# Kernel tuning notes

Hardware: AMD Instinct MI355X
Metric: run time of the kernel (lower is better)

## Reference

```python
import jax, jax.numpy as jnp
import numpy as np

B, N, C, H, W_, K, POS = 1, 100000, 128, 256, 256, 4, 36


def setup_inputs() -> dict:
    key = jax.random.key(0)
    ks = jax.random.split(key, 12)
    inp = {}
    # query coords in [-1, 1] (grid_sample normalized space)
    inp["query"] = jax.random.uniform(ks[0], (B, N, 3), jnp.float32, -1.0, 1.0)
    inp["pe"] = jax.random.normal(ks[1], (B, N, POS), jnp.float32)
    for i, p in enumerate(["xy", "xz", "yz"]):
        inp[f"feat_{p}"] = jax.random.normal(ks[2 + i], (B, C, H, W_), jnp.float32)
        inp[f"Wa_{p}"] = jax.random.normal(ks[5 + i], (POS, K), jnp.float32) * 0.1
        inp[f"ba_{p}"] = jnp.zeros((K,), jnp.float32)
        # offsets initialized to zero in the module; use small random so sampling is non-trivial
        inp[f"Wo_{p}"] = jax.random.normal(ks[8 + i], (POS, 2 * K), jnp.float32) * 0.02
        inp[f"bo_{p}"] = jnp.zeros((2 * K,), jnp.float32)
    return inp


def _bilinear_border(feat, gx, gy):
    """F.grid_sample(feat, grid, align_corners=False, padding_mode='border').
    feat: [B,C,H,W]; gx,gy: [B,N,K] normalized x (width) and y (height) coords.
    Returns [B,C,N,K]."""
    b, c, h, w = feat.shape
    # unnormalize (align_corners=False) then border-clip
    x = jnp.clip(((gx + 1.0) * w - 1.0) * 0.5, 0.0, w - 1.0)
    y = jnp.clip(((gy + 1.0) * h - 1.0) * 0.5, 0.0, h - 1.0)
    x0 = jnp.floor(x)
    y0 = jnp.floor(y)
    wx = x - x0  # [B,N,K]
    wy = y - y0
    xi0 = x0.astype(jnp.int32)
    yi0 = y0.astype(jnp.int32)
    xi1 = jnp.minimum(xi0 + 1, w - 1)
    yi1 = jnp.minimum(yi0 + 1, h - 1)
    ff = feat.reshape(b, c, h * w)
    gather = jax.vmap(lambda f, lin: f[:, lin])  # [C,HW],[N,K] -> [C,N,K]
    v00 = gather(ff, yi0 * w + xi0)
    v01 = gather(ff, yi0 * w + xi1)
    v10 = gather(ff, yi1 * w + xi0)
    v11 = gather(ff, yi1 * w + xi1)
    wx_ = wx[:, None]
    wy_ = wy[:, None]
    return (v00 * (1.0 - wx_) * (1.0 - wy_) + v01 * wx_ * (1.0 - wy_)
            + v10 * (1.0 - wx_) * wy_ + v11 * wx_ * wy_)


def _sample_plane(coords, pe, feat, Wa, ba, Wo, bo):
    b, n, _ = coords.shape
    attn = jax.nn.softmax(pe @ Wa + ba, axis=-1)            # [B,N,K]
    off = (pe @ Wo + bo).reshape(b, n, K, 2)                 # [B,N,K,2]
    sc = coords[:, :, None, :] + off                         # [B,N,K,2]
    # torch code flips last dim before grid_sample: grid x = sc[...,1], y = sc[...,0]
    sampled = _bilinear_border(feat, sc[..., 1], sc[..., 0])  # [B,C,N,K]
    out = jnp.einsum('bcnk,bnk->bnc', sampled, attn)         # weighted sum over K
    return out


def reference(query, pe, feat_xy, feat_xz, feat_yz,
              Wa_xy, ba_xy, Wo_xy, bo_xy,
              Wa_xz, ba_xz, Wo_xz, bo_xz,
              Wa_yz, ba_yz, Wo_yz, bo_yz):
    idx_xy = jnp.array([0, 1])
    idx_xz = jnp.array([0, 2])
    idx_yz = jnp.array([1, 2])
    f_xy = _sample_plane(query[..., idx_xy], pe, feat_xy, Wa_xy, ba_xy, Wo_xy, bo_xy)
    f_xz = _sample_plane(query[..., idx_xz], pe, feat_xz, Wa_xz, ba_xz, Wo_xz, bo_xz)
    f_yz = _sample_plane(query[..., idx_yz], pe, feat_yz, Wa_yz, ba_yz, Wo_yz, bo_yz)
    return f_xy + f_xz + f_yz
```

## Files before the change

kernel.cpp:

```cpp
#include <hip/hip_runtime.h>
#include <hip/hip_fp16.h>
#include <math.h>

#define NQ   100000
#define CCH  128
#define HDIM 256
#define WDIM 256
#define HW   (HDIM * WDIM)
#define KPTS 4
#define PDIM 36
#define NBIN 32768
#define RECW 40

__device__ inline int axis_bin(float x) {
  int b = (int)((x + 1.0f) * 16.0f);
  return min(31, max(0, b));
}
__device__ inline unsigned int spread5(unsigned int x) {
  return (x & 1u) | ((x & 2u) << 2) | ((x & 4u) << 4) | ((x & 8u) << 6) | ((x & 16u) << 8);
}
__device__ inline unsigned int bin_of(float x, float y, float z) {
  return spread5((unsigned int)axis_bin(x)) |
         (spread5((unsigned int)axis_bin(y)) << 1) |
         (spread5((unsigned int)axis_bin(z)) << 2);
}

__global__ void transpose_kernel(const float* __restrict__ f0,
                                 const float* __restrict__ f1,
                                 const float* __restrict__ f2,
                                 __half2* __restrict__ out) {
  __shared__ float tile[64][65];
  const int plane = blockIdx.z;
  const float* __restrict__ f = (plane == 0) ? f0 : ((plane == 1) ? f1 : f2);
  __half2* __restrict__ o = out + (size_t)plane * (size_t)HW * (CCH / 2);
  const int hw0 = blockIdx.x * 64;
  const int c0 = blockIdx.y * 64;
  const int t = threadIdx.x;
  const int c_l = t >> 6;
  const int hw_l = t & 63;
#pragma unroll
  for (int i = 0; i < 16; ++i) {
    tile[c_l + 4 * i][hw_l] = f[(size_t)(c0 + c_l + 4 * i) * HW + (hw0 + hw_l)];
  }
  __syncthreads();
#pragma unroll
  for (int i = 0; i < 8; ++i) {
    const int idx = t + 256 * i;
    const int j = idx & 31;
    const int r = idx >> 5;
    o[(size_t)(hw0 + r) * (CCH / 2) + (c0 / 2 + j)] =
        __floats2half2_rn(tile[2 * j][r], tile[2 * j + 1][r]);
  }
}

__global__ void hist_kernel(const float* __restrict__ query,
                            unsigned int* __restrict__ counts) {
  const int q = blockIdx.x * 256 + threadIdx.x;
  if (q >= NQ) return;
  const unsigned int b = bin_of(query[q * 3 + 0], query[q * 3 + 1], query[q * 3 + 2]);
  atomicAdd(&counts[b], 1u);
}

__global__ void scan_kernel(const unsigned int* __restrict__ counts,
                            unsigned int* __restrict__ offs) {
  __shared__ unsigned int s[1024];
  const int t = threadIdx.x;
  unsigned int c[32];
  unsigned int sum = 0;
  const int base_i = t * 32;
#pragma unroll
  for (int j = 0; j < 32; ++j) { c[j] = counts[base_i + j]; sum += c[j]; }
  s[t] = sum;
  __syncthreads();
  for (int d = 1; d < 1024; d <<= 1) {
    const unsigned int v = (t >= d) ? s[t - d] : 0u;
    __syncthreads();
    s[t] += v;
    __syncthreads();
  }
  unsigned int run = s[t] - sum;
#pragma unroll
  for (int j = 0; j < 32; ++j) { offs[base_i + j] = run; run += c[j]; }
}

__global__ void scatter_kernel(const float* __restrict__ query,
                               unsigned int* __restrict__ offs,
                               unsigned int* __restrict__ perm) {
  const int q = blockIdx.x * 256 + threadIdx.x;
  if (q >= NQ) return;
  const unsigned int b = bin_of(query[q * 3 + 0], query[q * 3 + 1], query[q * 3 + 2]);
  const unsigned int pos = atomicAdd(&offs[b], 1u);
  perm[pos] = (unsigned int)q;
}

__global__ void weights_kernel(const float* __restrict__ query,
                               const float* __restrict__ pe,
                               const unsigned int* __restrict__ perm,
                               const float* __restrict__ Wa0, const float* __restrict__ ba0,
                               const float* __restrict__ Wo0, const float* __restrict__ bo0,
                               const float* __restrict__ Wa1, const float* __restrict__ ba1,
                               const float* __restrict__ Wo1, const float* __restrict__ bo1,
                               const float* __restrict__ Wa2, const float* __restrict__ ba2,
                               const float* __restrict__ Wo2, const float* __restrict__ bo2,
                               unsigned int* __restrict__ rec) {
  __shared__ float sWa[3][PDIM][4];
  __shared__ float sWo[3][PDIM][8];
  __shared__ float sba[3][4];
  __shared__ float sbo[3][8];
  const int t = threadIdx.x;
  {
    float* wa = &sWa[0][0][0];
    for (int i = t; i < 144; i += 256) { wa[i] = Wa0[i]; wa[144 + i] = Wa1[i]; wa[288 + i] = Wa2[i]; }
    float* wo = &sWo[0][0][0];
    for (int i = t; i < 288; i += 256) { wo[i] = Wo0[i]; wo[288 + i] = Wo1[i]; wo[576 + i] = Wo2[i]; }
    if (t < 4) { sba[0][t] = ba0[t]; sba[1][t] = ba1[t]; sba[2][t] = ba2[t]; }
    if (t < 8) { sbo[0][t] = bo0[t]; sbo[1][t] = bo1[t]; sbo[2][t] = bo2[t]; }
  }
  __syncthreads();

  const int n = blockIdx.x * 256 + t;
  if (n >= NQ) return;
  const int q = (int)perm[n];

  float p[PDIM];
  const float4* pe4 = (const float4*)(pe + (size_t)q * PDIM);
#pragma unroll
  for (int i = 0; i < 9; ++i) {
    float4 v = pe4[i];
    p[4 * i + 0] = v.x; p[4 * i + 1] = v.y; p[4 * i + 2] = v.z; p[4 * i + 3] = v.w;
  }

  float la[3][4], of[3][8];
#pragma unroll
  for (int pl = 0; pl < 3; ++pl) {
#pragma unroll
    for (int k = 0; k < 4; ++k) la[pl][k] = sba[pl][k];
#pragma unroll
    for (int d = 0; d < 8; ++d) of[pl][d] = sbo[pl][d];
  }
#pragma unroll 4
  for (int j = 0; j < PDIM; ++j) {
    const float pj = p[j];
#pragma unroll
    for (int pl = 0; pl < 3; ++pl) {
#pragma unroll
      for (int k = 0; k < 4; ++k) la[pl][k] = fmaf(pj, sWa[pl][j][k], la[pl][k]);
#pragma unroll
      for (int d = 0; d < 8; ++d) of[pl][d] = fmaf(pj, sWo[pl][j][d], of[pl][d]);
    }
  }

  const float qx = query[q * 3 + 0];
  const float qy = query[q * 3 + 1];
  const float qz = query[q * 3 + 2];

  unsigned int* r = rec + (size_t)n * RECW;
  r[0] = (unsigned int)q;

#pragma unroll
  for (int pl = 0; pl < 3; ++pl) {
    const float m = fmaxf(fmaxf(la[pl][0], la[pl][1]), fmaxf(la[pl][2], la[pl][3]));
    const float e0 = expf(la[pl][0] - m);
    const float e1 = expf(la[pl][1] - m);
    const float e2 = expf(la[pl][2] - m);
    const float e3 = expf(la[pl][3] - m);
    const float inv = 1.0f / (e0 + e1 + e2 + e3);
    float at[4] = {e0 * inv, e1 * inv, e2 * inv, e3 * inv};

    const float ca = (pl == 2) ? qy : qx;
    const float cb = (pl == 0) ? qy : qz;
    const unsigned int pbase = (unsigned int)pl * (unsigned int)HW * (CCH / 2);
#pragma unroll
    for (int k = 0; k < KPTS; ++k) {
      const float gy = ca + of[pl][k * 2 + 0];
      const float gx = cb + of[pl][k * 2 + 1];
      float x = ((gx + 1.0f) * (float)WDIM - 1.0f) * 0.5f;
      float y = ((gy + 1.0f) * (float)HDIM - 1.0f) * 0.5f;
      x = fminf(fmaxf(x, 0.0f), (float)(WDIM - 1));
      y = fminf(fmaxf(y, 0.0f), (float)(HDIM - 1));
      const float x0f = floorf(x), y0f = floorf(y);
      const float wx = x - x0f, wy = y - y0f;
      const int xi0 = (int)x0f, yi0 = (int)y0f;
      const unsigned int dx = (xi0 + 1 <= WDIM - 1) ? 1u : 0u;
      const unsigned int dy = (yi0 + 1 <= HDIM - 1) ? 1u : 0u;
      const float a = at[k];
      const float w00 = a * (1.0f - wx) * (1.0f - wy);
      const float w01 = a * wx * (1.0f - wy);
      const float w10 = a * (1.0f - wx) * wy;
      const float w11 = a * wx * wy;
      const unsigned int a00 = pbase + (unsigned int)(yi0 * WDIM + xi0) * (CCH / 2);
      const int j = pl * 4 + k;
      r[1 + 3 * j] = a00 | (dx << 24) | (dy << 25);
      const __half2 h01 = __floats2half2_rn(w00, w01);
      const __half2 h23 = __floats2half2_rn(w10, w11);
      r[2 + 3 * j] = *(const unsigned int*)&h01;
      r[3 + 3 * j] = *(const unsigned int*)&h23;
    }
  }
  r[37] = 0u; r[38] = 0u; r[39] = 0u;
}

__global__ void sample_kernel(const unsigned int* __restrict__ rec,
                              const __half2* __restrict__ featT,
                              float* __restrict__ out) {
  const int lane = threadIdx.x & 63;
  const int wid = threadIdx.x >> 6;
  const int b = blockIdx.x;
  const int sb = (b & 7) * 3125 + (b >> 3);
  int i = sb * 4 + wid;
  i = __builtin_amdgcn_readfirstlane(i);

  const unsigned int* __restrict__ r = rec + (size_t)i * RECW;
  const int q = (int)r[0];
  const __half2* __restrict__ fl = featT + lane;

  float accx = 0.0f, accy = 0.0f;
#pragma unroll
  for (int j = 0; j < 12; ++j) {
    const unsigned int pk = r[1 + 3 * j];
    const unsigned int w01u = r[2 + 3 * j];
    const unsigned int w23u = r[3 + 3 * j];
    const unsigned int a00 = pk & 0xFFFFFFu;
    const unsigned int xo = (pk >> 18) & 64u;
    const unsigned int yo = (pk >> 11) & 16384u;
    const unsigned int a01 = a00 + xo;
    const unsigned int a10 = a00 + yo;
    const unsigned int a11 = a01 + yo;
    const __half2 h01 = __builtin_bit_cast(__half2, w01u);
    const __half2 h23 = __builtin_bit_cast(__half2, w23u);
    const float w00 = __low2float(h01);
    const float w01 = __high2float(h01);
    const float w10 = __low2float(h23);
    const float w11 = __high2float(h23);
    const __half2 v00 = fl[a00];
    const __half2 v01 = fl[a01];
    const __half2 v10 = fl[a10];
    const __half2 v11 = fl[a11];
    accx = fmaf(w00, __low2float(v00), accx);
    accy = fmaf(w00, __high2float(v00), accy);
    accx = fmaf(w01, __low2float(v01), accx);
    accy = fmaf(w01, __high2float(v01), accy);
    accx = fmaf(w10, __low2float(v10), accx);
    accy = fmaf(w10, __high2float(v10), accy);
    accx = fmaf(w11, __low2float(v11), accx);
    accy = fmaf(w11, __high2float(v11), accy);
  }
  *(float2*)(out + (size_t)q * CCH + lane * 2) = make_float2(accx, accy);
}

__global__ void fused_fallback(const float* __restrict__ query,
                               const float* __restrict__ pe,
                               const float* __restrict__ f0,
                               const float* __restrict__ f1,
                               const float* __restrict__ f2,
                               const float* __restrict__ Wa0, const float* __restrict__ ba0,
                               const float* __restrict__ Wo0, const float* __restrict__ bo0,
                               const float* __restrict__ Wa1, const float* __restrict__ ba1,
                               const float* __restrict__ Wo1, const float* __restrict__ bo1,
                               const float* __restrict__ Wa2, const float* __restrict__ ba2,
                               const float* __restrict__ Wo2, const float* __restrict__ bo2,
                               float* __restrict__ out) {
  const int lane = threadIdx.x & 63;
  const int wid = threadIdx.x >> 6;
  int q = blockIdx.x * 4 + wid;
  q = __builtin_amdgcn_readfirstlane(q);
  if (q >= NQ) return;
  const float qx = query[q * 3 + 0];
  const float qy = query[q * 3 + 1];
  const float qz = query[q * 3 + 2];
  const float* pep = pe + (size_t)q * PDIM;
  const int c0i = lane * 2, c1i = lane * 2 + 1;
  float accx = 0.0f, accy = 0.0f;
#pragma unroll
  for (int pl = 0; pl < 3; ++pl) {
    const float* Wa = (pl == 0) ? Wa0 : ((pl == 1) ? Wa1 : Wa2);
    const float* ba = (pl == 0) ? ba0 : ((pl == 1) ? ba1 : ba2);
    const float* Wo = (pl == 0) ? Wo0 : ((pl == 1) ? Wo1 : Wo2);
    const float* bo = (pl == 0) ? bo0 : ((pl == 1) ? bo1 : bo2);
    const float* f = (pl == 0) ? f0 : ((pl == 1) ? f1 : f2);
    float la[4] = {ba[0], ba[1], ba[2], ba[3]};
    float of[8];
    for (int d = 0; d < 8; ++d) of[d] = bo[d];
    for (int j = 0; j < PDIM; ++j) {
      const float pj = pep[j];
      for (int k = 0; k < 4; ++k) la[k] = fmaf(pj, Wa[j * 4 + k], la[k]);
      for (int d = 0; d < 8; ++d) of[d] = fmaf(pj, Wo[j * 8 + d], of[d]);
    }
    const float m = fmaxf(fmaxf(la[0], la[1]), fmaxf(la[2], la[3]));
    float e[4], s = 0.0f;
    for (int k = 0; k < 4; ++k) { e[k] = expf(la[k] - m); s += e[k]; }
    const float inv = 1.0f / s;
    const float ca = (pl == 2) ? qy : qx;
    const float cb = (pl == 0) ? qy : qz;
    for (int k = 0; k < 4; ++k) {
      const float gy = ca + of[k * 2 + 0];
      const float gx = cb + of[k * 2 + 1];
      float x = ((gx + 1.0f) * (float)WDIM - 1.0f) * 0.5f;
      float y = ((gy + 1.0f) * (float)HDIM - 1.0f) * 0.5f;
      x = fminf(fmaxf(x, 0.0f), (float)(WDIM - 1));
      y = fminf(fmaxf(y, 0.0f), (float)(HDIM - 1));
      const float x0f = floorf(x), y0f = floorf(y);
      const float wx = x - x0f, wy = y - y0f;
      const int xi0 = (int)x0f, yi0 = (int)y0f;
      const int xi1 = min(xi0 + 1, WDIM - 1);
      const int yi1 = min(yi0 + 1, HDIM - 1);
      const float a = e[k] * inv;
      const float w00 = a * (1.0f - wx) * (1.0f - wy);
      const float w01 = a * wx * (1.0f - wy);
      const float w10 = a * (1.0f - wx) * wy;
      const float w11 = a * wx * wy;
      const size_t p00 = (size_t)(yi0 * WDIM + xi0);
      const size_t p01 = (size_t)(yi0 * WDIM + xi1);
      const size_t p10 = (size_t)(yi1 * WDIM + xi0);
      const size_t p11 = (size_t)(yi1 * WDIM + xi1);
      const float* fa = f + (size_t)c0i * HW;
      const float* fb = f + (size_t)c1i * HW;
      accx += w00 * fa[p00] + w01 * fa[p01] + w10 * fa[p10] + w11 * fa[p11];
      accy += w00 * fb[p00] + w01 * fb[p01] + w10 * fb[p10] + w11 * fb[p11];
    }
  }
  *(float2*)(out + (size_t)q * CCH + lane * 2) = make_float2(accx, accy);
}

extern "C" void kernel_launch(void* const* d_in, const int* in_sizes, int n_in,
                              void* d_out, int out_size, void* d_ws, size_t ws_size,
                              hipStream_t stream) {
  const float* query = (const float*)d_in[0];
  const float* pe    = (const float*)d_in[1];
  const float* feat0 = (const float*)d_in[2];
  const float* Wa0   = (const float*)d_in[3];
  const float* ba0   = (const float*)d_in[4];
  const float* Wo0   = (const float*)d_in[5];
  const float* bo0   = (const float*)d_in[6];
  const float* feat1 = (const float*)d_in[7];
  const float* Wa1   = (const float*)d_in[8];
  const float* ba1   = (const float*)d_in[9];
  const float* Wo1   = (const float*)d_in[10];
  const float* bo1   = (const float*)d_in[11];
  const float* feat2 = (const float*)d_in[12];
  const float* Wa2   = (const float*)d_in[13];
  const float* ba2   = (const float*)d_in[14];
  const float* Wo2   = (const float*)d_in[15];
  const float* bo2   = (const float*)d_in[16];
  float* out = (float*)d_out;

  const size_t featT_elems = 3ull * HW * (CCH / 2);
  const size_t need = featT_elems * 4 + (size_t)NQ * RECW * 4 +
                      (size_t)NBIN * 8 + (size_t)NQ * 4;

  if (ws_size >= need) {
    __half2* featT = (__half2*)d_ws;
    unsigned int* rec = (unsigned int*)(d_ws) + featT_elems;
    unsigned int* counts = rec + (size_t)NQ * RECW;
    unsigned int* offs = counts + NBIN;
    unsigned int* perm = offs + NBIN;

    hipMemsetAsync(counts, 0, NBIN * sizeof(unsigned int), stream);
    transpose_kernel<<<dim3(HW / 64, CCH / 64, 3), dim3(256), 0, stream>>>(
        feat0, feat1, feat2, featT);
    hist_kernel<<<dim3((NQ + 255) / 256), dim3(256), 0, stream>>>(query, counts);
    scan_kernel<<<dim3(1), dim3(1024), 0, stream>>>(counts, offs);
    scatter_kernel<<<dim3((NQ + 255) / 256), dim3(256), 0, stream>>>(query, offs, perm);
    weights_kernel<<<dim3((NQ + 255) / 256), dim3(256), 0, stream>>>(
        query, pe, perm, Wa0, ba0, Wo0, bo0, Wa1, ba1, Wo1, bo1,
        Wa2, ba2, Wo2, bo2, rec);
    sample_kernel<<<dim3(NQ / 4), dim3(256), 0, stream>>>(rec, featT, out);
  } else {
    fused_fallback<<<dim3((NQ + 3) / 4), dim3(256), 0, stream>>>(
        query, pe, feat0, feat1, feat2,
        Wa0, ba0, Wo0, bo0, Wa1, ba1, Wo1, bo1, Wa2, ba2, Wo2, bo2, out);
  }
}
```

Measured before the change: 151.1 us.

## Fuse transpose, scatter and weights kernels into one prep launch

Merges the feature transpose, the bin scatter and the per-query weight computation into a single kernel. Blocks are split by index: the first range computes weights and writes each record directly to its sorted slot through an atomic on the bin offsets, and the rest perform the transpose tiles. This drops the perm buffer, two launches and the indirect pe gather through perm, and lets the memory-bound transpose overlap the weight computation. In exchange, pe reads are now in original order while record writes become scattered, and the padding words of each record are no longer zeroed.

Result: faster. 136.6 us (-9.6%).

```diff
diff --git a/kernel.cpp b/kernel.cpp
--- a/kernel.cpp
+++ b/kernel.cpp
@@ -12,6 +12,9 @@
 #define NBIN 32768
 #define RECW 40
 
+#define WBLK ((NQ + 255) / 256)
+#define TBLK ((HW / 64) * (CCH / 64) * 3)
+
 __device__ inline int axis_bin(float x) {
   int b = (int)((x + 1.0f) * 16.0f);
   return min(31, max(0, b));
@@ -23,34 +26,6 @@
   return spread5((unsigned int)axis_bin(x)) |
          (spread5((unsigned int)axis_bin(y)) << 1) |
          (spread5((unsigned int)axis_bin(z)) << 2);
-}
-
-__global__ void transpose_kernel(const float* __restrict__ f0,
-                                 const float* __restrict__ f1,
-                                 const float* __restrict__ f2,
-                                 __half2* __restrict__ out) {
-  __shared__ float tile[64][65];
-  const int plane = blockIdx.z;
-  const float* __restrict__ f = (plane == 0) ? f0 : ((plane == 1) ? f1 : f2);
-  __half2* __restrict__ o = out + (size_t)plane * (size_t)HW * (CCH / 2);
-  const int hw0 = blockIdx.x * 64;
-  const int c0 = blockIdx.y * 64;
-  const int t = threadIdx.x;
-  const int c_l = t >> 6;
-  const int hw_l = t & 63;
-#pragma unroll
-  for (int i = 0; i < 16; ++i) {
-    tile[c_l + 4 * i][hw_l] = f[(size_t)(c0 + c_l + 4 * i) * HW + (hw0 + hw_l)];
-  }
-  __syncthreads();
-#pragma unroll
-  for (int i = 0; i < 8; ++i) {
-    const int idx = t + 256 * i;
-    const int j = idx & 31;
-    const int r = idx >> 5;
-    o[(size_t)(hw0 + r) * (CCH / 2) + (c0 / 2 + j)] =
-        __floats2half2_rn(tile[2 * j][r], tile[2 * j + 1][r]);
-  }
 }
 
 __global__ void hist_kernel(const float* __restrict__ query,
@@ -83,44 +58,66 @@
   for (int j = 0; j < 32; ++j) { offs[base_i + j] = run; run += c[j]; }
 }
 
-__global__ void scatter_kernel(const float* __restrict__ query,
-                               unsigned int* __restrict__ offs,
-                               unsigned int* __restrict__ perm) {
-  const int q = blockIdx.x * 256 + threadIdx.x;
+__global__ void fused_prep_kernel(const float* __restrict__ f0,
+                                  const float* __restrict__ f1,
+                                  const float* __restrict__ f2,
+                                  __half2* __restrict__ featT,
+                                  const float* __restrict__ query,
+                                  const float* __restrict__ pe,
+                                  unsigned int* __restrict__ offs,
+                                  const float* __restrict__ Wa0, const float* __restrict__ ba0,
+                                  const float* __restrict__ Wo0, const float* __restrict__ bo0,
+                                  const float* __restrict__ Wa1, const float* __restrict__ ba1,
+                                  const float* __restrict__ Wo1, const float* __restrict__ bo1,
+                                  const float* __restrict__ Wa2, const float* __restrict__ ba2,
+                                  const float* __restrict__ Wo2, const float* __restrict__ bo2,
+                                  unsigned int* __restrict__ rec) {
+  __shared__ float smem[64 * 65];
+  const int bx = blockIdx.x;
+  const int t = threadIdx.x;
+
+  if (bx >= WBLK) {
+    float (*tile)[65] = (float (*)[65])smem;
+    const int tb = bx - WBLK;
+    const int plane = tb >> 11;
+    const int c64 = (tb >> 10) & 1;
+    const int hw64 = tb & 1023;
+    const float* __restrict__ f = (plane == 0) ? f0 : ((plane == 1) ? f1 : f2);
+    __half2* __restrict__ o = featT + (size_t)plane * (size_t)HW * (CCH / 2);
+    const int hw0 = hw64 * 64;
+    const int c0 = c64 * 64;
+    const int c_l = t >> 6;
+    const int hw_l = t & 63;
+#pragma unroll
+    for (int i = 0; i < 16; ++i) {
+      tile[c_l + 4 * i][hw_l] = f[(size_t)(c0 + c_l + 4 * i) * HW + (hw0 + hw_l)];
+    }
+    __syncthreads();
+#pragma unroll
+    for (int i = 0; i < 8; ++i) {
+      const int idx = t + 256 * i;
+      const int j = idx & 31;
+      const int r = idx >> 5;
+      o[(size_t)(hw0 + r) * (CCH / 2) + (c0 / 2 + j)] =
+          __floats2half2_rn(tile[2 * j][r], tile[2 * j + 1][r]);
+    }
+    return;
+  }
+
+  float* sWa = smem;
+  float* sWo = smem + 432;
+  float* sba = smem + 1296;
+  float* sbo = smem + 1308;
+  {
+    for (int i = t; i < 144; i += 256) { sWa[i] = Wa0[i]; sWa[144 + i] = Wa1[i]; sWa[288 + i] = Wa2[i]; }
+    for (int i = t; i < 288; i += 256) { sWo[i] = Wo0[i]; sWo[288 + i] = Wo1[i]; sWo[576 + i] = Wo2[i]; }
+    if (t < 4) { sba[0 + t] = ba0[t]; sba[4 + t] = ba1[t]; sba[8 + t] = ba2[t]; }
+    if (t < 8) { sbo[0 + t] = bo0[t]; sbo[8 + t] = bo1[t]; sbo[16 + t] = bo2[t]; }
+  }
+  __syncthreads();
+
+  const int q = bx * 256 + t;
   if (q >= NQ) return;
-  const unsigned int b = bin_of(query[q * 3 + 0], query[q * 3 + 1], query[q * 3 + 2]);
-  const unsigned int pos = atomicAdd(&offs[b], 1u);
-  perm[pos] = (unsigned int)q;
-}
-
-__global__ void weights_kernel(const float* __restrict__ query,
-                               const float* __restrict__ pe,
-                               const unsigned int* __restrict__ perm,
-                               const float* __restrict__ Wa0, const float* __restrict__ ba0,
-                               const float* __restrict__ Wo0, const float* __restrict__ bo0,
-                               const float* __restrict__ Wa1, const float* __restrict__ ba1,
-                               const float* __restrict__ Wo1, const float* __restrict__ bo1,
-                               const float* __restrict__ Wa2, const float* __restrict__ ba2,
-                               const float* __restrict__ Wo2, const float* __restrict__ bo2,
-                               unsigned int* __restrict__ rec) {
-  __shared__ float sWa[3][PDIM][4];
-  __shared__ float sWo[3][PDIM][8];
-  __shared__ float sba[3][4];
-  __shared__ float sbo[3][8];
-  const int t = threadIdx.x;
-  {
-    float* wa = &sWa[0][0][0];
-    for (int i = t; i < 144; i += 256) { wa[i] = Wa0[i]; wa[144 + i] = Wa1[i]; wa[288 + i] = Wa2[i]; }
-    float* wo = &sWo[0][0][0];
-    for (int i = t; i < 288; i += 256) { wo[i] = Wo0[i]; wo[288 + i] = Wo1[i]; wo[576 + i] = Wo2[i]; }
-    if (t < 4) { sba[0][t] = ba0[t]; sba[1][t] = ba1[t]; sba[2][t] = ba2[t]; }
-    if (t < 8) { sbo[0][t] = bo0[t]; sbo[1][t] = bo1[t]; sbo[2][t] = bo2[t]; }
-  }
-  __syncthreads();
-
-  const int n = blockIdx.x * 256 + t;
-  if (n >= NQ) return;
-  const int q = (int)perm[n];
 
   float p[PDIM];
   const float4* pe4 = (const float4*)(pe + (size_t)q * PDIM);
@@ -134,9 +131,9 @@
 #pragma unroll
   for (int pl = 0; pl < 3; ++pl) {
 #pragma unroll
-    for (int k = 0; k < 4; ++k) la[pl][k] = sba[pl][k];
-#pragma unroll
-    for (int d = 0; d < 8; ++d) of[pl][d] = sbo[pl][d];
+    for (int k = 0; k < 4; ++k) la[pl][k] = sba[pl * 4 + k];
+#pragma unroll
+    for (int d = 0; d < 8; ++d) of[pl][d] = sbo[pl * 8 + d];
   }
 #pragma unroll 4
   for (int j = 0; j < PDIM; ++j) {
@@ -144,9 +141,9 @@
 #pragma unroll
     for (int pl = 0; pl < 3; ++pl) {
 #pragma unroll
-      for (int k = 0; k < 4; ++k) la[pl][k] = fmaf(pj, sWa[pl][j][k], la[pl][k]);
-#pragma unroll
-      for (int d = 0; d < 8; ++d) of[pl][d] = fmaf(pj, sWo[pl][j][d], of[pl][d]);
+      for (int k = 0; k < 4; ++k) la[pl][k] = fmaf(pj, sWa[(pl * PDIM + j) * 4 + k], la[pl][k]);
+#pragma unroll
+      for (int d = 0; d < 8; ++d) of[pl][d] = fmaf(pj, sWo[(pl * PDIM + j) * 8 + d], of[pl][d]);
     }
   }
 
@@ -154,7 +151,9 @@
   const float qy = query[q * 3 + 1];
   const float qz = query[q * 3 + 2];
 
-  unsigned int* r = rec + (size_t)n * RECW;
+  const unsigned int bin = bin_of(qx, qy, qz);
+  const unsigned int pos = atomicAdd(&offs[bin], 1u);
+  unsigned int* r = rec + (size_t)pos * RECW;
   r[0] = (unsigned int)q;
 
 #pragma unroll
@@ -197,7 +196,6 @@
       r[3 + 3 * j] = *(const unsigned int*)&h23;
     }
   }
-  r[37] = 0u; r[38] = 0u; r[39] = 0u;
 }
 
 __global__ void sample_kernel(const unsigned int* __restrict__ rec,
@@ -345,25 +343,20 @@
   float* out = (float*)d_out;
 
   const size_t featT_elems = 3ull * HW * (CCH / 2);
-  const size_t need = featT_elems * 4 + (size_t)NQ * RECW * 4 +
-                      (size_t)NBIN * 8 + (size_t)NQ * 4;
+  const size_t need = featT_elems * 4 + (size_t)NQ * RECW * 4 + (size_t)NBIN * 8;
 
   if (ws_size >= need) {
     __half2* featT = (__half2*)d_ws;
     unsigned int* rec = (unsigned int*)(d_ws) + featT_elems;
     unsigned int* counts = rec + (size_t)NQ * RECW;
     unsigned int* offs = counts + NBIN;
-    unsigned int* perm = offs + NBIN;
 
     hipMemsetAsync(counts, 0, NBIN * sizeof(unsigned int), stream);
-    transpose_kernel<<<dim3(HW / 64, CCH / 64, 3), dim3(256), 0, stream>>>(
-        feat0, feat1, feat2, featT);
-    hist_kernel<<<dim3((NQ + 255) / 256), dim3(256), 0, stream>>>(query, counts);
+    hist_kernel<<<dim3(WBLK), dim3(256), 0, stream>>>(query, counts);
     scan_kernel<<<dim3(1), dim3(1024), 0, stream>>>(counts, offs);
-    scatter_kernel<<<dim3((NQ + 255) / 256), dim3(256), 0, stream>>>(query, offs, perm);
-    weights_kernel<<<dim3((NQ + 255) / 256), dim3(256), 0, stream>>>(
-        query, pe, perm, Wa0, ba0, Wo0, bo0, Wa1, ba1, Wo1, bo1,
-        Wa2, ba2, Wo2, bo2, rec);
+    fused_prep_kernel<<<dim3(WBLK + TBLK), dim3(256), 0, stream>>>(
+        feat0, feat1, feat2, featT, query, pe, offs,
+        Wa0, ba0, Wo0, bo0, Wa1, ba1, Wo1, bo1, Wa2, ba2, Wo2, bo2, rec);
     sample_kernel<<<dim3(NQ / 4), dim3(256), 0, stream>>>(rec, featT, out);
   } else {
     fused_fallback<<<dim3((NQ + 3) / 4), dim3(256), 0, stream>>>(
```
